# Performance work log

Measured on AMD Instinct MI355X. Metric: run time of the kernel, lower is better.

## Reference

```python
import jax, jax.numpy as jnp
import numpy as np

N = 6144
IN_FEATS = 512
OUT_FEATS = 64
NHEADS = 8
ALPHA = 0.2
NEG_BIG = -9e15


def setup_inputs() -> dict:
    key = jax.random.key(0)
    k_x, k_adj, k_w, k_a1, k_a2 = jax.random.split(key, 5)
    x = jax.random.normal(k_x, (N, IN_FEATS), dtype=jnp.float32)
    adj = jax.random.randint(k_adj, (N, N), 0, 2, dtype=jnp.int32)
    # xavier_uniform with gain=1.414 ~ sqrt(2)
    gain = 1.414
    bw = gain * np.sqrt(6.0 / (IN_FEATS + OUT_FEATS))
    W = jax.random.uniform(k_w, (NHEADS, IN_FEATS, OUT_FEATS), jnp.float32, -bw, bw)
    ba = gain * np.sqrt(6.0 / (OUT_FEATS + 1))
    a1 = jax.random.uniform(k_a1, (NHEADS, OUT_FEATS), jnp.float32, -ba, ba)
    a2 = jax.random.uniform(k_a2, (NHEADS, OUT_FEATS), jnp.float32, -ba, ba)
    return {"x": x, "adj": adj, "W": W, "a1": a1, "a2": a2}


def reference(x, adj, W, a1, a2):
    # h: [H, N, F] per-head projected features
    h = jnp.einsum("ni,hif->hnf", x, W)
    s1 = jnp.einsum("hnf,hf->hn", h, a1)  # [H, N]
    s2 = jnp.einsum("hnf,hf->hn", h, a2)  # [H, N]
    # outer-sum score [H, N, N], leaky-relu, adjacency mask, row softmax
    scores = jax.nn.leaky_relu(s1[:, :, None] + s2[:, None, :], negative_slope=ALPHA)
    scores = jnp.where(adj[None] > 0, scores, NEG_BIG)
    att = jax.nn.softmax(scores, axis=-1)
    out = jnp.einsum("hnm,hmf->hnf", att, h)  # [H, N, F]
    # concat heads: [N, H*F]
    out = jnp.transpose(out, (1, 0, 2)).reshape(N, NHEADS * OUT_FEATS)
    return jax.nn.elu(out)
```

## Files before the change

### kernel.cpp

```cpp
#include <hip/hip_runtime.h>
#include <hip/hip_bf16.h>
#include <stdint.h>

#define N_NODES 6144
#define IN_F    512
#define OUT_F   64
#define NH      8
#define ALPHA   0.2f
#define L2E     1.4426950408889634f
#define NTILES  (N_NODES / 64)

typedef __attribute__((ext_vector_type(8))) short bf16x8;
typedef __attribute__((ext_vector_type(8))) _Float16 f16x8;
typedef __attribute__((ext_vector_type(4))) float f32x4;

#define MFMA16B(a, b, c) __builtin_amdgcn_mfma_f32_16x16x32_bf16(a, b, c, 0, 0, 0)
#define MFMA16H(a, b, c) __builtin_amdgcn_mfma_f32_16x16x32_f16(a, b, c, 0, 0, 0)

__device__ __forceinline__ unsigned short f2bf(float f) {
    uint32_t u = __float_as_uint(f);
    u += 0x7fffu + ((u >> 16) & 1u);
    return (unsigned short)(u >> 16);
}
__device__ __forceinline__ float bf2f(unsigned short h) {
    return __uint_as_float(((uint32_t)h) << 16);
}
__device__ __forceinline__ unsigned short f16b(float f) {
    union { _Float16 h; unsigned short u; } c;
    c.h = (_Float16)f;
    return c.u;
}
__device__ __forceinline__ uint32_t encf(float x) {
    int i = __float_as_int(x);
    return (i >= 0) ? ((uint32_t)i | 0x80000000u) : ~(uint32_t)i;
}
__device__ __forceinline__ float decf(uint32_t u) {
    int i = (u & 0x80000000u) ? (int)(u & 0x7FFFFFFFu) : ~(int)u;
    return __int_as_float(i);
}

__global__ __launch_bounds__(256) void k_prep(
    const float* __restrict__ x, unsigned short* __restrict__ xh,
    unsigned short* __restrict__ xl,
    const float* __restrict__ W, unsigned short* __restrict__ wthF,
    unsigned short* __restrict__ wtlF, uint32_t* __restrict__ s2mu,
    const int* __restrict__ adj, unsigned long long* __restrict__ bmT)
{
    const int bid = blockIdx.x;
    if (bid < 2048) {
        const int lane = threadIdx.x & 63;
        const int wgid = bid * 4 + (threadIdx.x >> 6);
        for (int ch = wgid; ch < 96 * 96; ch += 8192) {
            const int cb = ch % 96, rblk = ch / 96;
            const int* ap = adj + (size_t)(rblk * 64) * N_NODES + cb * 64 + lane;
            unsigned long long keep = 0;
            for (int rr = 0; rr < 64; ++rr) {
                unsigned long long b = __ballot(ap[(size_t)rr * N_NODES] > 0);
                if (lane == rr) keep = b;
            }
            bmT[(size_t)cb * N_NODES + rblk * 64 + lane] = keep;
        }
    } else if (bid < 5120) {
        int i = (bid - 2048) * 256 + threadIdx.x;
        float4 v = ((const float4*)x)[i];
        float vv[4] = {v.x, v.y, v.z, v.w};
        unsigned short h4[4], l4[4];
#pragma unroll
        for (int c = 0; c < 4; ++c) {
            unsigned short hb = f2bf(vv[c]);
            h4[c] = hb;
            l4[c] = f2bf(vv[c] - bf2f(hb));
        }
        ((ushort4*)xh)[i] = make_ushort4(h4[0], h4[1], h4[2], h4[3]);
        ((ushort4*)xl)[i] = make_ushort4(l4[0], l4[1], l4[2], l4[3]);
    } else {
        int tid = (bid - 5120) * 256 + threadIdx.x;
        if (bid == 5120 && threadIdx.x < NH) s2mu[threadIdx.x] = 0u;
        int lane = tid & 63;
        int rest = tid >> 6;
        int ct = rest & 3;
        int i = (rest >> 2) & 15;
        int h = rest >> 6;
        int f = ct * 16 + (lane & 15);
        int k0 = i * 32 + (lane >> 4) * 8;
        unsigned short oh[8], ol[8];
#pragma unroll
        for (int e = 0; e < 8; ++e) {
            float wv = W[((size_t)h * IN_F + k0 + e) * OUT_F + f];
            unsigned short hb = f2bf(wv);
            oh[e] = hb;
            ol[e] = f2bf(wv - bf2f(hb));
        }
        ushort4* dh = (ushort4*)(wthF + (size_t)tid * 8);
        dh[0] = make_ushort4(oh[0], oh[1], oh[2], oh[3]);
        dh[1] = make_ushort4(oh[4], oh[5], oh[6], oh[7]);
        ushort4* dl = (ushort4*)(wtlF + (size_t)tid * 8);
        dl[0] = make_ushort4(ol[0], ol[1], ol[2], ol[3]);
        dl[1] = make_ushort4(ol[4], ol[5], ol[6], ol[7]);
    }
}

__global__ __launch_bounds__(256) void k_proj(
    const unsigned short* __restrict__ xh, const unsigned short* __restrict__ xl,
    const unsigned short* __restrict__ wthF, const unsigned short* __restrict__ wtlF,
    const float* __restrict__ a1, const float* __restrict__ a2,
    float* __restrict__ s1, float* __restrict__ s2,
    uint32_t* __restrict__ s2mu, unsigned short* __restrict__ hTF)
{
    __shared__ unsigned short hlds[64][64];

    const int head = blockIdx.x & 7;
    const int rb = blockIdx.x >> 3;
    const int w = threadIdx.x >> 6;
    const int lane = threadIdx.x & 63;
    const int r15 = lane & 15;
    const int g = lane >> 4;
    const int rowbase = rb * 64 + w * 16;
    const int rowA = rowbase + r15;

    f32x4 acc[4] = {};
    const unsigned short* xhp = xh + (size_t)rowA * IN_F + g * 8;
    const unsigned short* xlp = xl + (size_t)rowA * IN_F + g * 8;
    const unsigned short* wb = wthF + ((size_t)head * 16 * 4 * 64) * 8 + lane * 8;
    const unsigned short* wl = wtlF + ((size_t)head * 16 * 4 * 64) * 8 + lane * 8;

#pragma unroll 4
    for (int i = 0; i < 16; ++i) {
        const int k0 = i * 32;
        bf16x8 ah = *(const bf16x8*)(xhp + k0);
        bf16x8 al = *(const bf16x8*)(xlp + k0);
#pragma unroll
        for (int ct = 0; ct < 4; ++ct) {
            const size_t fo = (size_t)(i * 4 + ct) * 512;
            bf16x8 bh = *(const bf16x8*)(wb + fo);
            bf16x8 bl = *(const bf16x8*)(wl + fo);
            acc[ct] = MFMA16B(ah, bh, acc[ct]);
            acc[ct] = MFMA16B(ah, bl, acc[ct]);
            acc[ct] = MFMA16B(al, bh, acc[ct]);
        }
    }

    float a1v[4], a2v[4];
#pragma unroll
    for (int ct = 0; ct < 4; ++ct) {
        a1v[ct] = a1[head * 64 + ct * 16 + r15];
        a2v[ct] = a2[head * 64 + ct * 16 + r15];
    }
    float sp1[4] = {0, 0, 0, 0}, sp2[4] = {0, 0, 0, 0};
#pragma unroll
    for (int ct = 0; ct < 4; ++ct)
#pragma unroll
        for (int j = 0; j < 4; ++j) {
            sp1[j] += acc[ct][j] * a1v[ct];
            sp2[j] += acc[ct][j] * a2v[ct];
        }
#pragma unroll
    for (int d = 1; d < 16; d <<= 1) {
#pragma unroll
        for (int j = 0; j < 4; ++j) {
            sp1[j] += __shfl_xor(sp1[j], d);
            sp2[j] += __shfl_xor(sp2[j], d);
        }
    }
    if (r15 == 0) {
#pragma unroll
        for (int j = 0; j < 4; ++j) {
            int n = rowbase + g * 4 + j;
            s1[head * N_NODES + n] = sp1[j];
            s2[head * N_NODES + n] = sp2[j];
        }
    }
    {
        float m = fmaxf(fmaxf(sp2[0], sp2[1]), fmaxf(sp2[2], sp2[3]));
        m = fmaxf(m, __shfl_xor(m, 16));
        m = fmaxf(m, __shfl_xor(m, 32));
        if (lane == 0) atomicMax(s2mu + head, encf(m));
    }

#pragma unroll
    for (int ct = 0; ct < 4; ++ct) {
        ushort4 pk;
        pk.x = f16b(acc[ct][0]);
        pk.y = f16b(acc[ct][1]);
        pk.z = f16b(acc[ct][2]);
        pk.w = f16b(acc[ct][3]);
        int f_l = ct * 16 + r15;
        int n0 = w * 16 + g * 4;
        int col = (((n0 >> 3) ^ (f_l & 7)) << 3) + (n0 & 7);
        *(ushort4*)&hlds[f_l][col] = pk;
    }
    __syncthreads();

#pragma unroll
    for (int q = 0; q < 2; ++q) {
        int fid = 2 * w + q;
        int wk = fid >> 2, ct = fid & 3;
        int f_l = ct * 16 + (lane & 15);
        int nch = wk * 4 + (lane >> 4);
        int col = ((nch ^ (f_l & 7)) << 3);
        int4 v = *(const int4*)&hlds[f_l][col];
        size_t base = (((size_t)(head * 96 + rb)) * 8 + fid) * 512 + lane * 8;
        *(int4*)(hTF + base) = v;
    }
}

__device__ __forceinline__ f16x8 mk_pa16(int4 ep, int4 en, uint32_t e1p2,
                                         uint32_t e1n2, uint32_t ms,
                                         uint32_t kFFFF)
{
    const uint32_t epw[4] = {(uint32_t)ep.x, (uint32_t)ep.y, (uint32_t)ep.z,
                             (uint32_t)ep.w};
    const uint32_t enw[4] = {(uint32_t)en.x, (uint32_t)en.y, (uint32_t)en.z,
                             (uint32_t)en.w};
    union { uint32_t u[4]; f16x8 v; } r;
#define PAIR(J, B0, B1)                                                       \
    {                                                                         \
        uint32_t pa, pb, pm, mw;                                              \
        asm("v_pk_mul_f16 %0, %1, %2" : "=v"(pa) : "v"(e1p2), "v"(epw[J]));   \
        asm("v_pk_mul_f16 %0, %1, %2" : "=v"(pb) : "v"(e1n2), "v"(enw[J]));   \
        asm("v_pk_max_f16 %0, %1, %2" : "=v"(pm) : "v"(pa), "v"(pb));         \
        uint32_t mb0, mb1;                                                    \
        asm("v_bfe_i32 %0, %1, " #B0 ", 1" : "=v"(mb0) : "v"(ms));            \
        asm("v_bfe_i32 %0, %1, " #B1 ", 1" : "=v"(mb1) : "v"(ms));            \
        asm("v_bfi_b32 %0, %1, %2, %3"                                        \
            : "=v"(mw) : "s"(kFFFF), "v"(mb0), "v"(mb1));                     \
        r.u[J] = pm & mw;                                                     \
    }
    PAIR(0, 0, 1)
    PAIR(1, 2, 3)
    PAIR(2, 4, 5)
    PAIR(3, 6, 7)
#undef PAIR
    return r.v;
}

struct Ph {
    int4 hb0, hb1, hb2, hb3;
};
struct Pm {
    uint32_t m0, m1;
};

__device__ __forceinline__ f16x8 as_f16x8(int4 v) {
    union { int4 i; f16x8 h; } c;
    c.i = v;
    return c.h;
}

__global__ __launch_bounds__(256, 3) void k_flash(
    const unsigned short* __restrict__ hTF, const float* __restrict__ s1,
    const float* __restrict__ s2, const uint32_t* __restrict__ s2mu,
    const uint32_t* __restrict__ bmT32, float* __restrict__ out)
{
    __shared__ uint32_t epL[3072];
    __shared__ uint32_t enL[3072];
    __shared__ float fs[128 * 20];

    const int head = blockIdx.x & 7;
    const int rb = blockIdx.x >> 3;
    const int tid = threadIdx.x;
    const int w = tid >> 6, lane = tid & 63, r15 = lane & 15, g = lane >> 4;
    const int w01 = w & 1;
    const int wk = w >> 1;
    const int shg = g * 8;
    const uint32_t kFFFF = 0xFFFFu;

    const float s2mh = decf(s2mu[head]);
    {
        const float4* s2h = (const float4*)(s2 + head * N_NODES);
#pragma unroll
        for (int i0 = 0; i0 < 6; ++i0) {
            int i = tid + i0 * 256;
            float4 v = s2h[i];
            uint32_t p0 = f16b(exp2f((v.x - s2mh) * L2E));
            uint32_t p1 = f16b(exp2f((v.y - s2mh) * L2E));
            uint32_t p2 = f16b(exp2f((v.z - s2mh) * L2E));
            uint32_t p3 = f16b(exp2f((v.w - s2mh) * L2E));
            uint32_t n0 = f16b(exp2f(ALPHA * (v.x - s2mh) * L2E));
            uint32_t n1 = f16b(exp2f(ALPHA * (v.y - s2mh) * L2E));
            uint32_t n2 = f16b(exp2f(ALPHA * (v.z - s2mh) * L2E));
            uint32_t n3 = f16b(exp2f(ALPHA * (v.w - s2mh) * L2E));
            epL[2 * i] = p0 | (p1 << 16);
            epL[2 * i + 1] = p2 | (p3 << 16);
            enL[2 * i] = n0 | (n1 << 16);
            enL[2 * i + 1] = n2 | (n3 << 16);
        }
    }

    const int rA = rb * 64 + w01 * 32 + r15;
    const int rB = rA + 16;
    const float s1A = s1[head * N_NODES + rA];
    const float s1B = s1[head * N_NODES + rB];
    const float t0A = s1A + s2mh, t0B = s1B + s2mh;
    const float MrA = fmaxf(t0A, ALPHA * t0A);
    const float MrB = fmaxf(t0B, ALPHA * t0B);
    uint32_t E1pA2, E1nA2, E1pB2, E1nB2;
    {
        uint32_t a = f16b(exp2f((t0A - MrA) * L2E));
        uint32_t b = f16b(exp2f((ALPHA * t0A - MrA) * L2E));
        uint32_t c = f16b(exp2f((t0B - MrB) * L2E));
        uint32_t d = f16b(exp2f((ALPHA * t0B - MrB) * L2E));
        E1pA2 = a | (a << 16);
        E1nA2 = b | (b << 16);
        E1pB2 = c | (c << 16);
        E1nB2 = d | (d << 16);
    }

    const unsigned short* hp = hTF +
        ((size_t)(head * 96) * 8 + wk * 4) * 512 + lane * 8;
    const uint32_t* pa = bmT32 + (size_t)rA * 2 + wk;

    const uint32_t* __restrict__ epb = epL + wk * 16 + g * 4;
    const uint32_t* __restrict__ enb = enL + wk * 16 + g * 4;

    f32x4 accA[4] = {}, accB[4] = {};
    f32x4 accSA = {}, accSB = {};
    const f16x8 vones = {(_Float16)1.0f, (_Float16)1.0f, (_Float16)1.0f,
                         (_Float16)1.0f, (_Float16)1.0f, (_Float16)1.0f,
                         (_Float16)1.0f, (_Float16)1.0f};

    __syncthreads();

    auto loadH = [&](Ph& P) {
        asm volatile("global_load_dwordx4 %0, %1, off"
                     : "=v"(P.hb0) : "v"(hp));
        asm volatile("global_load_dwordx4 %0, %1, off offset:1024"
                     : "=v"(P.hb1) : "v"(hp));
        asm volatile("global_load_dwordx4 %0, %1, off offset:2048"
                     : "=v"(P.hb2) : "v"(hp));
        asm volatile("global_load_dwordx4 %0, %1, off offset:3072"
                     : "=v"(P.hb3) : "v"(hp));
        hp += 4096;
    };
    auto loadM = [&](Pm& P) {
        asm volatile("global_load_dword %0, %1, off"
                     : "=v"(P.m0) : "v"(pa));
        asm volatile("global_load_dword %0, %1, off offset:128"
                     : "=v"(P.m1) : "v"(pa));
        pa += 12288;
    };
    auto compute = [&](int t, Ph& H, Pm& M) {
        int4 ep = *(const int4*)(epb + t * 32);
        int4 en = *(const int4*)(enb + t * 32);
        f16x8 paA = mk_pa16(ep, en, E1pA2, E1nA2, M.m0 >> shg, kFFFF);
        f16x8 paB = mk_pa16(ep, en, E1pB2, E1nB2, M.m1 >> shg, kFFFF);
        __builtin_amdgcn_s_setprio(1);
        accSA = MFMA16H(paA, vones, accSA);
        accSB = MFMA16H(paB, vones, accSB);
        f16x8 h0 = as_f16x8(H.hb0), h1 = as_f16x8(H.hb1);
        f16x8 h2 = as_f16x8(H.hb2), h3 = as_f16x8(H.hb3);
        accA[0] = MFMA16H(paA, h0, accA[0]);
        accB[0] = MFMA16H(paB, h0, accB[0]);
        accA[1] = MFMA16H(paA, h1, accA[1]);
        accB[1] = MFMA16H(paB, h1, accB[1]);
        accA[2] = MFMA16H(paA, h2, accA[2]);
        accB[2] = MFMA16H(paB, h2, accB[2]);
        accA[3] = MFMA16H(paA, h3, accA[3]);
        accB[3] = MFMA16H(paB, h3, accB[3]);
        __builtin_amdgcn_s_setprio(0);
    };

    Ph H0, H1, H2;
    Pm M0, M1, M2, M3, M4, M5;
    loadM(M0);
    loadM(M1);
    loadM(M2);
    loadH(H0);
    loadM(M3);
    loadH(H1);
    loadM(M4);
    loadH(H2);
    loadM(M5);

#define PHASE(K, HH, MM)                                                      \
    asm volatile("s_waitcnt vmcnt(14)");                                      \
    __builtin_amdgcn_sched_barrier(0);                                        \
    compute(t + K, HH, MM);                                                   \
    loadH(HH);                                                                \
    loadM(MM);

    for (int t = 0; t < NTILES; t += 6) {
        PHASE(0, H0, M0)
        PHASE(1, H1, M1)
        PHASE(2, H2, M2)
        PHASE(3, H0, M3)
        PHASE(4, H1, M4)
        PHASE(5, H2, M5)
    }
#undef PHASE
    asm volatile("s_waitcnt vmcnt(0)");
    __builtin_amdgcn_sched_barrier(0);

    const int slot = w01 * 64 + lane;
    const int fcb = head * 64;
    const int nA = rb * 64 + w01 * 32 + g * 4;

    if (wk == 1) {
#pragma unroll
        for (int ct = 0; ct < 4; ++ct)
#pragma unroll
            for (int j = 0; j < 4; ++j) fs[slot * 20 + ct * 4 + j] = accA[ct][j];
#pragma unroll
        for (int j = 0; j < 4; ++j) fs[slot * 20 + 16 + j] = accSA[j];
    }
    __syncthreads();
    if (wk == 0) {
        float rinv[4];
#pragma unroll
        for (int j = 0; j < 4; ++j)
            rinv[j] = 1.0f / (accSA[j] + fs[slot * 20 + 16 + j]);
#pragma unroll
        for (int ct = 0; ct < 4; ++ct)
#pragma unroll
            for (int j = 0; j < 4; ++j) {
                float v = (accA[ct][j] + fs[slot * 20 + ct * 4 + j]) * rinv[j];
                v = (v > 0.f) ? v : (expf(v) - 1.f);
                out[(size_t)(nA + j) * 512 + fcb + ct * 16 + r15] = v;
            }
    }
    __syncthreads();
    if (wk == 1) {
#pragma unroll
        for (int ct = 0; ct < 4; ++ct)
#pragma unroll
            for (int j = 0; j < 4; ++j) fs[slot * 20 + ct * 4 + j] = accB[ct][j];
#pragma unroll
        for (int j = 0; j < 4; ++j) fs[slot * 20 + 16 + j] = accSB[j];
    }
    __syncthreads();
    if (wk == 0) {
        float rinv[4];
#pragma unroll
        for (int j = 0; j < 4; ++j)
            rinv[j] = 1.0f / (accSB[j] + fs[slot * 20 + 16 + j]);
#pragma unroll
        for (int ct = 0; ct < 4; ++ct)
#pragma unroll
            for (int j = 0; j < 4; ++j) {
                float v = (accB[ct][j] + fs[slot * 20 + ct * 4 + j]) * rinv[j];
                v = (v > 0.f) ? v : (expf(v) - 1.f);
                out[(size_t)(nA + 16 + j) * 512 + fcb + ct * 16 + r15] = v;
            }
    }
}

extern "C" void kernel_launch(void* const* d_in, const int* in_sizes, int n_in,
                              void* d_out, int out_size, void* d_ws, size_t ws_size,
                              hipStream_t stream)
{
    const float* x = (const float*)d_in[0];
    const int* adj = (const int*)d_in[1];
    const float* W = (const float*)d_in[2];
    const float* a1 = (const float*)d_in[3];
    const float* a2 = (const float*)d_in[4];
    float* out = (float*)d_out;

    char* ws = (char*)d_ws;
    size_t off = 0;
    auto take = [&](size_t bytes) {
        void* p = ws + off;
        off = (off + bytes + 255) & ~(size_t)255;
        return p;
    };
    unsigned short* xh   = (unsigned short*)take((size_t)N_NODES * IN_F * 2);
    unsigned short* xl   = (unsigned short*)take((size_t)N_NODES * IN_F * 2);
    unsigned short* wthF = (unsigned short*)take((size_t)512 * 512 * 2);
    unsigned short* wtlF = (unsigned short*)take((size_t)512 * 512 * 2);
    unsigned short* hTF  = (unsigned short*)take(
        (size_t)NH * 64 * N_NODES * 2 + 32768);
    float* s1  = (float*)take((size_t)NH * N_NODES * 4);
    float* s2  = (float*)take((size_t)NH * N_NODES * 4);
    uint32_t* s2mu = (uint32_t*)take(256);
    unsigned long long* bmT = (unsigned long long*)take(
        (size_t)N_NODES * (N_NODES / 64) * 8 + 393216);

    k_prep<<<dim3(5248), dim3(256), 0, stream>>>(
        x, xh, xl, W, wthF, wtlF, s2mu, adj, bmT);
    k_proj<<<dim3(NH * (N_NODES / 64)), dim3(256), 0, stream>>>(
        xh, xl, wthF, wtlF, a1, a2, s1, s2, s2mu, hTF);
    k_flash<<<dim3(NH * NTILES), dim3(256), 0, stream>>>(
        hTF, s1, s2, s2mu, (const uint32_t*)bmT, out);
}
```

Baseline: 156.8 us.

## Give each flash wave all 64 rows to halve H-tile loads per block

Measured after the change: 167.3 us. +6.7%, slower.

```diff
diff --git a/kernel.cpp b/kernel.cpp
--- a/kernel.cpp
+++ b/kernel.cpp
@@ -238,7 +238,7 @@
     int4 hb0, hb1, hb2, hb3;
 };
 struct Pm {
-    uint32_t m0, m1;
+    uint32_t m0, m1, m2, m3;
 };
 
 __device__ __forceinline__ f16x8 as_f16x8(int4 v) {
@@ -247,21 +247,20 @@
     return c.h;
 }
 
-__global__ __launch_bounds__(256, 3) void k_flash(
+__global__ __launch_bounds__(128, 2) void k_flash(
     const unsigned short* __restrict__ hTF, const float* __restrict__ s1,
     const float* __restrict__ s2, const uint32_t* __restrict__ s2mu,
     const uint32_t* __restrict__ bmT32, float* __restrict__ out)
 {
     __shared__ uint32_t epL[3072];
     __shared__ uint32_t enL[3072];
-    __shared__ float fs[128 * 20];
+    __shared__ float fs[64 * 40];
 
     const int head = blockIdx.x & 7;
     const int rb = blockIdx.x >> 3;
     const int tid = threadIdx.x;
-    const int w = tid >> 6, lane = tid & 63, r15 = lane & 15, g = lane >> 4;
-    const int w01 = w & 1;
-    const int wk = w >> 1;
+    const int wk = tid >> 6;
+    const int lane = tid & 63, r15 = lane & 15, g = lane >> 4;
     const int shg = g * 8;
     const uint32_t kFFFF = 0xFFFFu;
 
@@ -269,8 +268,8 @@
     {
         const float4* s2h = (const float4*)(s2 + head * N_NODES);
 #pragma unroll
-        for (int i0 = 0; i0 < 6; ++i0) {
-            int i = tid + i0 * 256;
+        for (int i0 = 0; i0 < 12; ++i0) {
+            int i = tid + i0 * 128;
             float4 v = s2h[i];
             uint32_t p0 = f16b(exp2f((v.x - s2mh) * L2E));
             uint32_t p1 = f16b(exp2f((v.y - s2mh) * L2E));
@@ -287,34 +286,27 @@
         }
     }
 
-    const int rA = rb * 64 + w01 * 32 + r15;
-    const int rB = rA + 16;
-    const float s1A = s1[head * N_NODES + rA];
-    const float s1B = s1[head * N_NODES + rB];
-    const float t0A = s1A + s2mh, t0B = s1B + s2mh;
-    const float MrA = fmaxf(t0A, ALPHA * t0A);
-    const float MrB = fmaxf(t0B, ALPHA * t0B);
-    uint32_t E1pA2, E1nA2, E1pB2, E1nB2;
-    {
-        uint32_t a = f16b(exp2f((t0A - MrA) * L2E));
-        uint32_t b = f16b(exp2f((ALPHA * t0A - MrA) * L2E));
-        uint32_t c = f16b(exp2f((t0B - MrB) * L2E));
-        uint32_t d = f16b(exp2f((ALPHA * t0B - MrB) * L2E));
-        E1pA2 = a | (a << 16);
-        E1nA2 = b | (b << 16);
-        E1pB2 = c | (c << 16);
-        E1nB2 = d | (d << 16);
+    uint32_t E1p2[4], E1n2[4];
+#pragma unroll
+    for (int rg = 0; rg < 4; ++rg) {
+        float s1r = s1[head * N_NODES + rb * 64 + rg * 16 + r15];
+        float t0 = s1r + s2mh;
+        float Mr = fmaxf(t0, ALPHA * t0);
+        uint32_t a = f16b(exp2f((t0 - Mr) * L2E));
+        uint32_t b = f16b(exp2f((ALPHA * t0 - Mr) * L2E));
+        E1p2[rg] = a | (a << 16);
+        E1n2[rg] = b | (b << 16);
     }
 
     const unsigned short* hp = hTF +
         ((size_t)(head * 96) * 8 + wk * 4) * 512 + lane * 8;
-    const uint32_t* pa = bmT32 + (size_t)rA * 2 + wk;
+    const uint32_t* pa = bmT32 + (size_t)(rb * 64 + r15) * 2 + wk;
 
     const uint32_t* __restrict__ epb = epL + wk * 16 + g * 4;
     const uint32_t* __restrict__ enb = enL + wk * 16 + g * 4;
 
-    f32x4 accA[4] = {}, accB[4] = {};
-    f32x4 accSA = {}, accSB = {};
+    f32x4 acc[4][4] = {};
+    f32x4 accS[4] = {};
     const f16x8 vones = {(_Float16)1.0f, (_Float16)1.0f, (_Float16)1.0f,
                          (_Float16)1.0f, (_Float16)1.0f, (_Float16)1.0f,
                          (_Float16)1.0f, (_Float16)1.0f};
@@ -337,110 +329,102 @@
                      : "=v"(P.m0) : "v"(pa));
         asm volatile("global_load_dword %0, %1, off offset:128"
                      : "=v"(P.m1) : "v"(pa));
+        asm volatile("global_load_dword %0, %1, off offset:256"
+                     : "=v"(P.m2) : "v"(pa));
+        asm volatile("global_load_dword %0, %1, off offset:384"
+                     : "=v"(P.m3) : "v"(pa));
         pa += 12288;
     };
     auto compute = [&](int t, Ph& H, Pm& M) {
         int4 ep = *(const int4*)(epb + t * 32);
         int4 en = *(const int4*)(enb + t * 32);
-        f16x8 paA = mk_pa16(ep, en, E1pA2, E1nA2, M.m0 >> shg, kFFFF);
-        f16x8 paB = mk_pa16(ep, en, E1pB2, E1nB2, M.m1 >> shg, kFFFF);
+        f16x8 pa0 = mk_pa16(ep, en, E1p2[0], E1n2[0], M.m0 >> shg, kFFFF);
+        f16x8 pa1 = mk_pa16(ep, en, E1p2[1], E1n2[1], M.m1 >> shg, kFFFF);
+        f16x8 pa2 = mk_pa16(ep, en, E1p2[2], E1n2[2], M.m2 >> shg, kFFFF);
+        f16x8 pa3 = mk_pa16(ep, en, E1p2[3], E1n2[3], M.m3 >> shg, kFFFF);
         __builtin_amdgcn_s_setprio(1);
-        accSA = MFMA16H(paA, vones, accSA);
-        accSB = MFMA16H(paB, vones, accSB);
+        accS[0] = MFMA16H(pa0, vones, accS[0]);
+        accS[1] = MFMA16H(pa1, vones, accS[1]);
+        accS[2] = MFMA16H(pa2, vones, accS[2]);
+        accS[3] = MFMA16H(pa3, vones, accS[3]);
         f16x8 h0 = as_f16x8(H.hb0), h1 = as_f16x8(H.hb1);
         f16x8 h2 = as_f16x8(H.hb2), h3 = as_f16x8(H.hb3);
-        accA[0] = MFMA16H(paA, h0, accA[0]);
-        accB[0] = MFMA16H(paB, h0, accB[0]);
-        accA[1] = MFMA16H(paA, h1, accA[1]);
-        accB[1] = MFMA16H(paB, h1, accB[1]);
-        accA[2] = MFMA16H(paA, h2, accA[2]);
-        accB[2] = MFMA16H(paB, h2, accB[2]);
-        accA[3] = MFMA16H(paA, h3, accA[3]);
-        accB[3] = MFMA16H(paB, h3, accB[3]);
+#define PVROW(RG, PA)                                                         \
+        acc[RG][0] = MFMA16H(PA, h0, acc[RG][0]);                             \
+        acc[RG][1] = MFMA16H(PA, h1, acc[RG][1]);                             \
+        acc[RG][2] = MFMA16H(PA, h2, acc[RG][2]);                             \
+        acc[RG][3] = MFMA16H(PA, h3, acc[RG][3]);
+        PVROW(0, pa0)
+        PVROW(1, pa1)
+        PVROW(2, pa2)
+        PVROW(3, pa3)
+#undef PVROW
         __builtin_amdgcn_s_setprio(0);
     };
 
-    Ph H0, H1, H2;
-    Pm M0, M1, M2, M3, M4, M5;
+    Ph H0, H1;
+    Pm M0, M1;
+    loadH(H0);
     loadM(M0);
+    loadH(H1);
     loadM(M1);
-    loadM(M2);
-    loadH(H0);
-    loadM(M3);
-    loadH(H1);
-    loadM(M4);
-    loadH(H2);
-    loadM(M5);
-
-#define PHASE(K, HH, MM)                                                      \
-    asm volatile("s_waitcnt vmcnt(14)");                                      \
-    __builtin_amdgcn_sched_barrier(0);                                        \
-    compute(t + K, HH, MM);                                                   \
-    loadH(HH);                                                                \
-    loadM(MM);
-
-    for (int t = 0; t < NTILES; t += 6) {
-        PHASE(0, H0, M0)
-        PHASE(1, H1, M1)
-        PHASE(2, H2, M2)
-        PHASE(3, H0, M3)
-        PHASE(4, H1, M4)
-        PHASE(5, H2, M5)
-    }
-#undef PHASE
+    for (int t = 0; t < NTILES; t += 2) {
+        asm volatile("s_waitcnt vmcnt(8)");
+        __builtin_amdgcn_sched_barrier(0);
+        compute(t, H0, M0);
+        loadH(H0);
+        loadM(M0);
+
+        asm volatile("s_waitcnt vmcnt(8)");
+        __builtin_amdgcn_sched_barrier(0);
+        compute(t + 1, H1, M1);
+        loadH(H1);
+        loadM(M1);
+    }
     asm volatile("s_waitcnt vmcnt(0)");
     __builtin_amdgcn_sched_barrier(0);
 
-    const int slot = w01 * 64 + lane;
     const int fcb = head * 64;
-    const int nA = rb * 64 + w01 * 32 + g * 4;
-
-    if (wk == 1) {
-#pragma unroll
-        for (int ct = 0; ct < 4; ++ct)
-#pragma unroll
-            for (int j = 0; j < 4; ++j) fs[slot * 20 + ct * 4 + j] = accA[ct][j];
-#pragma unroll
-        for (int j = 0; j < 4; ++j) fs[slot * 20 + 16 + j] = accSA[j];
-    }
-    __syncthreads();
-    if (wk == 0) {
-        float rinv[4];
-#pragma unroll
-        for (int j = 0; j < 4; ++j)
-            rinv[j] = 1.0f / (accSA[j] + fs[slot * 20 + 16 + j]);
-#pragma unroll
-        for (int ct = 0; ct < 4; ++ct)
-#pragma unroll
-            for (int j = 0; j < 4; ++j) {
-                float v = (accA[ct][j] + fs[slot * 20 + ct * 4 + j]) * rinv[j];
-                v = (v > 0.f) ? v : (expf(v) - 1.f);
-                out[(size_t)(nA + j) * 512 + fcb + ct * 16 + r15] = v;
+#pragma unroll
+    for (int ph = 0; ph < 2; ++ph) {
+        if (wk == 1) {
+#pragma unroll
+            for (int q = 0; q < 2; ++q) {
+                const int rg = ph * 2 + q;
+#pragma unroll
+                for (int ct = 0; ct < 4; ++ct)
+#pragma unroll
+                    for (int j = 0; j < 4; ++j)
+                        fs[lane * 40 + q * 20 + ct * 4 + j] = acc[rg][ct][j];
+#pragma unroll
+                for (int j = 0; j < 4; ++j)
+                    fs[lane * 40 + q * 20 + 16 + j] = accS[rg][j];
             }
-    }
-    __syncthreads();
-    if (wk == 1) {
-#pragma unroll
-        for (int ct = 0; ct < 4; ++ct)
-#pragma unroll
-            for (int j = 0; j < 4; ++j) fs[slot * 20 + ct * 4 + j] = accB[ct][j];
-#pragma unroll
-        for (int j = 0; j < 4; ++j) fs[slot * 20 + 16 + j] = accSB[j];
-    }
-    __syncthreads();
-    if (wk == 0) {
-        float rinv[4];
-#pragma unroll
-        for (int j = 0; j < 4; ++j)
-            rinv[j] = 1.0f / (accSB[j] + fs[slot * 20 + 16 + j]);
-#pragma unroll
-        for (int ct = 0; ct < 4; ++ct)
-#pragma unroll
-            for (int j = 0; j < 4; ++j) {
-                float v = (accB[ct][j] + fs[slot * 20 + ct * 4 + j]) * rinv[j];
-                v = (v > 0.f) ? v : (expf(v) - 1.f);
-                out[(size_t)(nA + 16 + j) * 512 + fcb + ct * 16 + r15] = v;
+        }
+        __syncthreads();
+        if (wk == 0) {
+#pragma unroll
+            for (int q = 0; q < 2; ++q) {
+                const int rg = ph * 2 + q;
+                float rinv[4];
+#pragma unroll
+                for (int j = 0; j < 4; ++j)
+                    rinv[j] = 1.0f /
+                        (accS[rg][j] + fs[lane * 40 + q * 20 + 16 + j]);
+                const int nA = rb * 64 + rg * 16 + g * 4;
+#pragma unroll
+                for (int ct = 0; ct < 4; ++ct)
+#pragma unroll
+                    for (int j = 0; j < 4; ++j) {
+                        float v = (acc[rg][ct][j] +
+                                   fs[lane * 40 + q * 20 + ct * 4 + j]) *
+                                  rinv[j];
+                        v = (v > 0.f) ? v : (expf(v) - 1.f);
+                        out[(size_t)(nA + j) * 512 + fcb + ct * 16 + r15] = v;
+                    }
             }
+        }
+        __syncthreads();
     }
 }
 
@@ -478,6 +462,6 @@
         x, xh, xl, W, wthF, wtlF, s2mu, adj, bmT);
     k_proj<<<dim3(NH * (N_NODES / 64)), dim3(256), 0, stream>>>(
         xh, xl, wthF, wtlF, a1, a2, s1, s2, s2mu, hTF);
-    k_flash<<<dim3(NH * NTILES), dim3(256), 0, stream>>>(
+    k_flash<<<dim3(NH * NTILES), dim3(128), 0, stream>>>(
         hTF, s1, s2, s2mu, (const uint32_t*)bmT, out);
 }
```
